# Kernel tuning notes

Measured on AMD Instinct MI355X. Metric: run time of the kernel, lower is better.

## Reference

```python
import jax, jax.numpy as jnp
import numpy as np

N, E, B, D, F_IN, E_IN, H = 8192, 32768, 256, 64, 11, 5, 128


def setup_inputs() -> dict:
    key = jax.random.key(0)
    ks = jax.random.split(key, 32)
    rn = lambda k, shape, s: jax.random.normal(k, shape, jnp.float32) * s
    inp = {
        'x': jax.random.normal(ks[0], (N, F_IN), jnp.float32),
        'edge_attr': jax.random.uniform(ks[1], (E, E_IN), jnp.float32),
        'lin0_w': rn(ks[2], (D, F_IN), 0.3), 'lin0_b': jnp.zeros((D,), jnp.float32),
        'nn1_w': rn(ks[3], (H, E_IN), 0.4), 'nn1_b': jnp.zeros((H,), jnp.float32),
        'nn2_w': rn(ks[4], (D * D, H), 0.05), 'nn2_b': jnp.zeros((D * D,), jnp.float32),
        'root_w': rn(ks[5], (D, D), 0.125), 'conv_b': jnp.zeros((D,), jnp.float32),
        'gru_w_ih': rn(ks[6], (3 * D, D), 0.125), 'gru_w_hh': rn(ks[7], (3 * D, D), 0.125),
        'gru_b_ih': jnp.zeros((3 * D,), jnp.float32), 'gru_b_hh': jnp.zeros((3 * D,), jnp.float32),
        's2s_w_ih': rn(ks[8], (4 * D, 2 * D), 0.1), 's2s_w_hh': rn(ks[9], (4 * D, D), 0.125),
        's2s_b_ih': jnp.zeros((4 * D,), jnp.float32), 's2s_b_hh': jnp.zeros((4 * D,), jnp.float32),
        'lin1_w': rn(ks[10], (D, 2 * D), 0.1), 'lin1_b': jnp.zeros((D,), jnp.float32),
        'lin2_w': rn(ks[11], (1, D), 0.125), 'lin2_b': jnp.zeros((1,), jnp.float32),
        'edge_index': jax.random.randint(ks[12], (2, E), 0, N),
        'batch': jnp.sort(jax.random.randint(ks[13], (N,), 0, B)),
    }
    return inp


def _forward(x, edge_attr, lin0_w, lin0_b, nn1_w, nn1_b, nn2_w, nn2_b, root_w, conv_b,
             gru_w_ih, gru_w_hh, gru_b_ih, gru_b_hh, s2s_w_ih, s2s_w_hh, s2s_b_ih, s2s_b_hh,
             lin1_w, lin1_b, lin2_w, lin2_b, edge_index, batch):
    src, dst = edge_index[0], edge_index[1]
    # edge-conditioned weights: MLP(edge_attr) -> [E, D, D]; edge_attr is fixed,
    # so compute once (identical math to calling conv.nn each iteration)
    W_e = (jax.nn.relu(edge_attr @ nn1_w.T + nn1_b) @ nn2_w.T + nn2_b).reshape(E, D, D)
    deg = jax.ops.segment_sum(jnp.ones((E,), jnp.float32), dst, num_segments=N)
    inv_deg = jnp.where(deg > 0, 1.0 / jnp.maximum(deg, 1.0), 0.0)[:, None]  # [N,1]

    out = jax.nn.relu(x @ lin0_w.T + lin0_b)  # [N, D]
    h = out
    for _ in range(3):
        # NNConv: gather src features, per-edge matmul, scatter-mean to dst, + root + bias
        msg = jnp.einsum('ed,edf->ef', out[src], W_e)  # [E, D]
        agg = jax.ops.segment_sum(msg, dst, num_segments=N) * inv_deg
        m = jax.nn.relu(agg + out @ root_w.T + conv_b)
        # single-step GRU (torch GRU equations)
        gx = m @ gru_w_ih.T + gru_b_ih
        gh = h @ gru_w_hh.T + gru_b_hh
        xr, xz, xn = jnp.split(gx, 3, axis=-1)
        hr, hz, hn = jnp.split(gh, 3, axis=-1)
        r = jax.nn.sigmoid(xr + hr)
        z = jax.nn.sigmoid(xz + hz)
        n = jnp.tanh(xn + r * hn)
        h = (1.0 - z) * n + z * h
        out = h

    # Set2Set pooling, 3 processing steps
    qh = jnp.zeros((B, D), jnp.float32)
    qc = jnp.zeros((B, D), jnp.float32)
    q_star = jnp.zeros((B, 2 * D), jnp.float32)
    for _ in range(3):
        gates = q_star @ s2s_w_ih.T + s2s_b_ih + qh @ s2s_w_hh.T + s2s_b_hh
        gi, gf, gg, go = jnp.split(gates, 4, axis=-1)
        qc = jax.nn.sigmoid(gf) * qc + jax.nn.sigmoid(gi) * jnp.tanh(gg)
        qh = jax.nn.sigmoid(go) * jnp.tanh(qc)
        q = qh  # [B, D]
        e = jnp.sum(out * q[batch], axis=-1)  # [N]
        emax = jax.ops.segment_max(e, batch, num_segments=B)
        emax = jnp.where(jnp.isfinite(emax), emax, 0.0)
        a = jnp.exp(e - emax[batch])
        a_sum = jax.ops.segment_sum(a, batch, num_segments=B)
        a = a / jnp.maximum(a_sum, 1e-12)[batch]
        r_vec = jax.ops.segment_sum(a[:, None] * out, batch, num_segments=B)  # [B, D]
        q_star = jnp.concatenate([q, r_vec], axis=-1)

    y = jax.nn.relu(q_star @ lin1_w.T + lin1_b) @ lin2_w.T + lin2_b
    return y.reshape(-1)  # [B]


def reference(x, edge_attr, lin0_w, lin0_b, nn1_w, nn1_b, nn2_w, nn2_b, root_w, conv_b,
              gru_w_ih, gru_w_hh, gru_b_ih, gru_b_hh, s2s_w_ih, s2s_w_hh, s2s_b_ih, s2s_b_hh,
              lin1_w, lin1_b, lin2_w, lin2_b, edge_index, batch):
    return _forward(x, edge_attr, lin0_w, lin0_b, nn1_w, nn1_b, nn2_w, nn2_b, root_w, conv_b,
                    gru_w_ih, gru_w_hh, gru_b_ih, gru_b_hh, s2s_w_ih, s2s_w_hh, s2s_b_ih, s2s_b_hh,
                    lin1_w, lin1_b, lin2_w, lin2_b, edge_index, batch)
```

## Files before the change

### kernel.cpp

```cpp
#include <hip/hip_runtime.h>
#include <hip/hip_bf16.h>
#include <stdint.h>

#define NN 8192
#define EE 32768
#define BB 256
#define DD 64
#define FIN 11
#define EIN 5
#define HH 128

typedef __attribute__((ext_vector_type(4))) float f32x4;
typedef __attribute__((ext_vector_type(8))) short bf16x8;

__device__ __forceinline__ float sigmoidf_(float x) { return 1.0f / (1.0f + expf(-x)); }

__device__ __forceinline__ void gload16(const void* g, void* l) {
    __builtin_amdgcn_global_load_lds(
        (const __attribute__((address_space(1))) unsigned int*)g,
        (__attribute__((address_space(3))) unsigned int*)l, 16, 0, 0);
}

__global__ __launch_bounds__(256) void k_cast(const float* __restrict__ src,
                                              __hip_bfloat16* __restrict__ dst) {
    int i = (blockIdx.x * 256 + threadIdx.x) * 4;
    float4 v = *(const float4*)(src + i);
    ushort4 o;
    __hip_bfloat16 b0 = __float2bfloat16(v.x); o.x = *(ushort*)&b0;
    __hip_bfloat16 b1 = __float2bfloat16(v.y); o.y = *(ushort*)&b1;
    __hip_bfloat16 b2 = __float2bfloat16(v.z); o.z = *(ushort*)&b2;
    __hip_bfloat16 b3 = __float2bfloat16(v.w); o.w = *(ushort*)&b3;
    *(ushort4*)((ushort*)dst + i) = o;
}

__global__ __launch_bounds__(256) void k_prep(const float* __restrict__ root_w,
                                              const float* __restrict__ whh,
                                              const float* __restrict__ bhh,
                                              const float* __restrict__ nn2b,
                                              float* __restrict__ Bcat,
                                              float* __restrict__ bcat) {
    int i = blockIdx.x * 256 + threadIdx.x;
    int r = i >> 6, c = i & 63;
    float v;
    if (r < 64) v = root_w[i];
    else if (r < 256) v = whh[(size_t)(r - 64) * 64 + c];
    else v = nn2b[c * 64 + (r - 256)];
    Bcat[i] = v;
    if (c == 0) bcat[r] = (r >= 64 && r < 256) ? bhh[r - 64] : 0.0f;
}

__global__ __launch_bounds__(256) void k_tw(const float* __restrict__ wih,
                                            const float* __restrict__ whh,
                                            float* __restrict__ wihT,
                                            float* __restrict__ whhT) {
    int i = blockIdx.x * 256 + threadIdx.x;
    if (i < 256 * 128) {
        int j = i >> 7, k = i & 127;
        wihT[k * 256 + j] = wih[i];
    } else {
        int i2 = i - 256 * 128;
        if (i2 < 256 * 64) {
            int j = i2 >> 6, k = i2 & 63;
            whhT[k * 256 + j] = whh[i2];
        }
    }
}

__global__ __launch_bounds__(256) void k_lin0(const float* __restrict__ x,
                                              const float* __restrict__ w,
                                              const float* __restrict__ b,
                                              float* __restrict__ out) {
    int idx = blockIdx.x * 256 + threadIdx.x;
    int n = idx >> 6, d = idx & 63;
    float a = b[d];
#pragma unroll
    for (int k = 0; k < FIN; k++) a += x[n * FIN + k] * w[d * FIN + k];
    out[idx] = fmaxf(a, 0.0f);
}

__global__ __launch_bounds__(256) void k_h1(const float* __restrict__ ea,
                                            const float* __restrict__ w,
                                            const float* __restrict__ b,
                                            __hip_bfloat16* __restrict__ h1) {
    int idx = blockIdx.x * 256 + threadIdx.x;
    int e = idx >> 7, k = idx & 127;
    float a = b[k];
#pragma unroll
    for (int j = 0; j < EIN; j++) a += ea[e * EIN + j] * w[k * EIN + j];
    h1[idx] = __float2bfloat16(fmaxf(a, 0.0f));
}

__global__ __launch_bounds__(256) void k_counts(const int* __restrict__ ei,
                                                const int* __restrict__ batch,
                                                int* __restrict__ deg,
                                                int* __restrict__ cnt) {
    int i = blockIdx.x * 256 + threadIdx.x;
    if (i < EE) atomicAdd(&deg[ei[EE + i]], 1);
    if (i < NN) atomicAdd(&cnt[batch[i]], 1);
}
__global__ __launch_bounds__(256) void k_inv(const int* __restrict__ deg, float* __restrict__ invd) {
    int n = blockIdx.x * 256 + threadIdx.x;
    if (n < NN) { int d = deg[n]; invd[n] = d > 0 ? 1.0f / (float)d : 0.0f; }
}
__global__ __launch_bounds__(256) void k_scan(const int* __restrict__ cnt, int* __restrict__ offs) {
    __shared__ int s[256];
    int t = threadIdx.x;
    s[t] = cnt[t];
    __syncthreads();
    for (int off = 1; off < 256; off <<= 1) {
        int v = (t >= off) ? s[t - off] : 0;
        __syncthreads();
        s[t] += v;
        __syncthreads();
    }
    offs[t + 1] = s[t];
    if (t == 0) offs[0] = 0;
}

__global__ __launch_bounds__(256) void k_wemsg(const __hip_bfloat16* __restrict__ h1,
                                               const __hip_bfloat16* __restrict__ nn2bf,
                                               const float* __restrict__ outN,
                                               const float* __restrict__ rgh,
                                               const int* __restrict__ ei,
                                               const float* __restrict__ invd,
                                               float* __restrict__ agg) {
    __shared__ ushort sB[2][64 * 128];
    __shared__ float soT[64 * 64];
    __shared__ float snbT[64 * 64];
    __shared__ int sDst[64];
    __shared__ float sIv[64];

    const int t = threadIdx.x;
    const int w = t >> 6, l = t & 63;
    const int q = l >> 4, l15 = l & 15;
    const int e0 = blockIdx.x * 64;

    {
        int r = t >> 2, seg = t & 3;
        int s_ = ei[e0 + r];
        const float* orow = outN + (size_t)s_ * 64 + seg * 16;
        const float* nrow = rgh + (size_t)s_ * 320 + 256 + seg * 16;
#pragma unroll
        for (int i = 0; i < 4; i++) {
            float4 v = *(const float4*)(orow + i * 4);
            float4 nb = *(const float4*)(nrow + i * 4);
            int c0 = seg * 16 + i * 4;
            soT[(c0 + 0) * 64 + r] = v.x;
            soT[(c0 + 1) * 64 + r] = v.y;
            soT[(c0 + 2) * 64 + r] = v.z;
            soT[(c0 + 3) * 64 + r] = v.w;
            snbT[(c0 + 0) * 64 + r] = nb.x;
            snbT[(c0 + 1) * 64 + r] = nb.y;
            snbT[(c0 + 2) * 64 + r] = nb.z;
            snbT[(c0 + 3) * 64 + r] = nb.w;
        }
        if (seg == 0) {
            int d_ = ei[EE + e0 + r];
            sDst[r] = d_;
            sIv[r] = invd[d_];
        }
    }
    bf16x8 af[4][4];
#pragma unroll
    for (int mi = 0; mi < 4; mi++)
#pragma unroll
        for (int kk = 0; kk < 4; kk++)
            af[mi][kk] = *(const bf16x8*)(h1 + (size_t)(e0 + mi * 16 + l15) * 128 + (kk * 4 + q) * 8);

#pragma unroll
    for (int i = 0; i < 4; i++) {
        int u = i * 256 + t;
        int r = u >> 4, c = u & 15, cs = c ^ (r & 7);
        gload16(nn2bf + ((size_t)r * 128 + cs * 8), &sB[0][(i * 256 + w * 64) * 8]);
    }
    __syncthreads();

    float msg[4][4];
#pragma unroll
    for (int mi = 0; mi < 4; mi++)
#pragma unroll
        for (int j = 0; j < 4; j++) msg[mi][j] = 0.0f;

    for (int d = 0; d < 64; ++d) {
        const int cur = d & 1;
        if (d < 63) {
#pragma unroll
            for (int i = 0; i < 4; i++) {
                int u = i * 256 + t;
                int r = u >> 4, c = u & 15, cs = c ^ (r & 7);
                gload16(nn2bf + ((size_t)((d + 1) * 64 + r) * 128 + cs * 8),
                        &sB[cur ^ 1][(i * 256 + w * 64) * 8]);
            }
        }
        const ushort* sbc = &sB[cur][0];
        f32x4 acc[4];
#pragma unroll
        for (int mi = 0; mi < 4; mi++) acc[mi] = (f32x4)0.0f;
        const int rb = w * 16 + l15;
#pragma unroll
        for (int kk = 0; kk < 4; kk++) {
            bf16x8 bfr = *(const bf16x8*)&sbc[(rb * 16 + ((kk * 4 + q) ^ (rb & 7))) * 8];
#pragma unroll
            for (int mi = 0; mi < 4; mi++)
                acc[mi] = __builtin_amdgcn_mfma_f32_16x16x32_bf16(af[mi][kk], bfr, acc[mi], 0, 0, 0);
        }
#pragma unroll
        for (int mi = 0; mi < 4; mi++) {
            f32x4 sov = *(const f32x4*)&soT[d * 64 + mi * 16 + q * 4];
#pragma unroll
            for (int j = 0; j < 4; j++) msg[mi][j] += acc[mi][j] * sov[j];
        }
        __syncthreads();
    }

#pragma unroll
    for (int mi = 0; mi < 4; mi++) {
        f32x4 nb = *(const f32x4*)&snbT[(w * 16 + l15) * 64 + mi * 16 + q * 4];
#pragma unroll
        for (int j = 0; j < 4; j++) {
            int er = mi * 16 + q * 4 + j;
            atomicAdd(&agg[(size_t)sDst[er] * 64 + w * 16 + l15], (msg[mi][j] + nb[j]) * sIv[er]);
        }
    }
}

__global__ __launch_bounds__(256) void k_rgh(const float* __restrict__ A,
                                             const float* __restrict__ Bm,
                                             const float* __restrict__ bias,
                                             float* __restrict__ C,
                                             float* __restrict__ aggz) {
    const int tid = threadIdx.x;
    const int bx = blockIdx.x, by = blockIdx.y;
    {
        int bid = by * 5 + bx;
        if (bid < 512) {
            float4 z; z.x = z.y = z.z = z.w = 0.0f;
            *(float4*)(aggz + (size_t)bid * 1024 + tid * 4) = z;
        }
    }
    __shared__ float sA[64 * 68];
    __shared__ float sB[64 * 68];
    const float* Ab = A + (size_t)by * 64 * 64;
    const float* Bb = Bm + (size_t)bx * 64 * 64;
    for (int fi = tid; fi < 64 * 16; fi += 256) {
        int r = fi >> 4, c = (fi & 15) * 4;
        *(float4*)&sA[r * 68 + c] = *(const float4*)(Ab + (size_t)r * 64 + c);
        *(float4*)&sB[r * 68 + c] = *(const float4*)(Bb + (size_t)r * 64 + c);
    }
    __syncthreads();
    const int tx = tid & 15, ty = tid >> 4;
    float acc[4][4];
#pragma unroll
    for (int i = 0; i < 4; i++)
#pragma unroll
        for (int j = 0; j < 4; j++) acc[i][j] = 0.0f;
    for (int k = 0; k < 64; k += 4) {
        float4 av[4], bv[4];
#pragma unroll
        for (int i = 0; i < 4; i++) av[i] = *(const float4*)&sA[(ty + 16 * i) * 68 + k];
#pragma unroll
        for (int j = 0; j < 4; j++) bv[j] = *(const float4*)&sB[(tx + 16 * j) * 68 + k];
#pragma unroll
        for (int i = 0; i < 4; i++)
#pragma unroll
            for (int j = 0; j < 4; j++) {
                acc[i][j] += av[i].x * bv[j].x;
                acc[i][j] += av[i].y * bv[j].y;
                acc[i][j] += av[i].z * bv[j].z;
                acc[i][j] += av[i].w * bv[j].w;
            }
    }
#pragma unroll
    for (int i = 0; i < 4; i++) {
        size_t row = (size_t)by * 64 + ty + 16 * i;
#pragma unroll
        for (int j = 0; j < 4; j++) {
            int col = bx * 64 + tx + 16 * j;
            C[row * 320 + col] = acc[i][j] + bias[col];
        }
    }
}

__global__ __launch_bounds__(256) void k_gxgru(const float* __restrict__ agg,
                                               const float* __restrict__ rgh,
                                               const float* __restrict__ cb,
                                               const float* __restrict__ wih,
                                               const float* __restrict__ bih,
                                               float* __restrict__ outN) {
    __shared__ float sA[64 * 68];
    __shared__ float sB[192 * 68];
    const int t = threadIdx.x;
    const int by = blockIdx.x;
    for (int fi = t; fi < 64 * 16; fi += 256) {
        int r = fi >> 4, c = (fi & 15) * 4;
        float4 av = *(const float4*)(agg + (size_t)(by * 64 + r) * 64 + c);
        float4 rv = *(const float4*)(rgh + (size_t)(by * 64 + r) * 320 + c);
        float4 cv = *(const float4*)(cb + c);
        float4 m;
        m.x = fmaxf(av.x + rv.x + cv.x, 0.0f);
        m.y = fmaxf(av.y + rv.y + cv.y, 0.0f);
        m.z = fmaxf(av.z + rv.z + cv.z, 0.0f);
        m.w = fmaxf(av.w + rv.w + cv.w, 0.0f);
        *(float4*)&sA[r * 68 + c] = m;
    }
    for (int fi = t; fi < 192 * 16; fi += 256) {
        int r = fi >> 4, c = (fi & 15) * 4;
        *(float4*)&sB[r * 68 + c] = *(const float4*)(wih + (size_t)r * 64 + c);
    }
    __syncthreads();
    const int tx = t & 15, ty = t >> 4;
    float acc[3][4][4];
#pragma unroll
    for (int cx = 0; cx < 3; cx++)
#pragma unroll
        for (int i = 0; i < 4; i++)
#pragma unroll
            for (int j = 0; j < 4; j++) acc[cx][i][j] = 0.0f;
    for (int k = 0; k < 64; k += 4) {
        float4 av[4];
#pragma unroll
        for (int i = 0; i < 4; i++) av[i] = *(const float4*)&sA[(ty + 16 * i) * 68 + k];
#pragma unroll
        for (int cx = 0; cx < 3; cx++) {
            float4 bv[4];
#pragma unroll
            for (int j = 0; j < 4; j++) bv[j] = *(const float4*)&sB[(cx * 64 + tx + 16 * j) * 68 + k];
#pragma unroll
            for (int i = 0; i < 4; i++)
#pragma unroll
                for (int j = 0; j < 4; j++) {
                    acc[cx][i][j] += av[i].x * bv[j].x;
                    acc[cx][i][j] += av[i].y * bv[j].y;
                    acc[cx][i][j] += av[i].z * bv[j].z;
                    acc[cx][i][j] += av[i].w * bv[j].w;
                }
        }
    }
#pragma unroll
    for (int i = 0; i < 4; i++) {
        int n = by * 64 + ty + 16 * i;
        const float* ghr = rgh + (size_t)n * 320 + 64;
#pragma unroll
        for (int j = 0; j < 4; j++) {
            int d = tx + 16 * j;
            float r = sigmoidf_(acc[0][i][j] + bih[d] + ghr[d]);
            float z = sigmoidf_(acc[1][i][j] + bih[64 + d] + ghr[64 + d]);
            float nn_ = tanhf(acc[2][i][j] + bih[128 + d] + r * ghr[128 + d]);
            float hp = outN[(size_t)n * 64 + d];
            outN[(size_t)n * 64 + d] = (1.0f - z) * nn_ + z * hp;
        }
    }
}

__global__ __launch_bounds__(256) void k_s2sall(const float* __restrict__ outN,
                                                const int* __restrict__ offs,
                                                const float* __restrict__ wihT,
                                                const float* __restrict__ whhT,
                                                const float* __restrict__ bih,
                                                const float* __restrict__ bhh,
                                                const float* __restrict__ lin1_w,
                                                const float* __restrict__ lin1_b,
                                                const float* __restrict__ lin2_w,
                                                const float* __restrict__ lin2_b,
                                                float* __restrict__ earr,
                                                float* __restrict__ y) {
    const int b = blockIdx.x, t = threadIdx.x;
    const int w = t >> 6, l = t & 63;
    __shared__ float qs[128], qhL[64], qcL[64], gates[256];
    __shared__ float red[8];
    __shared__ float rpart[4][64];
    __shared__ float hbuf[64];
    const int s0 = offs[b], s1 = offs[b + 1];
    if (t < 128) qs[t] = 0.0f;
    if (t < 64) { qhL[t] = 0.0f; qcL[t] = 0.0f; }
    __syncthreads();

    for (int st = 0; st < 3; st++) {
        float g = bih[t] + bhh[t];
        for (int k = 0; k < 128; k++) g += qs[k] * wihT[k * 256 + t];
        for (int k = 0; k < 64; k++) g += qhL[k] * whhT[k * 256 + t];
        gates[t] = g;
        __syncthreads();
        if (t < 64) {
            float gi = gates[t], gf = gates[64 + t], gg = gates[128 + t], go = gates[192 + t];
            float c = sigmoidf_(gf) * qcL[t] + sigmoidf_(gi) * tanhf(gg);
            qcL[t] = c;
            qhL[t] = sigmoidf_(go) * tanhf(c);
        }
        __syncthreads();
        float mx = -INFINITY;
        for (int i = s0 + w; i < s1; i += 4) {
            float p = outN[(size_t)i * 64 + l] * qhL[l];
#pragma unroll
            for (int o = 32; o > 0; o >>= 1) p += __shfl_xor(p, o, 64);
            if (l == 0) earr[i] = p;
            mx = fmaxf(mx, p);
        }
        if (l == 0) red[w] = mx;
        __syncthreads();
        mx = fmaxf(fmaxf(red[0], red[1]), fmaxf(red[2], red[3]));
        if (!isfinite(mx)) mx = 0.0f;
        float sm = 0.0f, racc = 0.0f;
        for (int i = s0 + w; i < s1; i += 4) {
            float a = expf(earr[i] - mx);
            sm += a;
            racc += a * outN[(size_t)i * 64 + l];
        }
        rpart[w][l] = racc;
        if (l == 0) red[4 + w] = sm;
        __syncthreads();
        float smT = fmaxf(red[4] + red[5] + red[6] + red[7], 1e-12f);
        if (t < 64) {
            float r = (rpart[0][t] + rpart[1][t] + rpart[2][t] + rpart[3][t]) / smT;
            qs[t] = qhL[t];
            qs[64 + t] = r;
        }
        __syncthreads();
    }
    if (t < 64) {
        float h = lin1_b[t];
        for (int k = 0; k < 128; k++) h += qs[k] * lin1_w[t * 128 + k];
        hbuf[t] = fmaxf(h, 0.0f) * lin2_w[t];
    }
    __syncthreads();
    if (w == 0) {
        float p = hbuf[l];
#pragma unroll
        for (int o = 32; o > 0; o >>= 1) p += __shfl_xor(p, o, 64);
        if (l == 0) y[b] = p + lin2_b[0];
    }
}

extern "C" void kernel_launch(void* const* d_in, const int* in_sizes, int n_in,
                              void* d_out, int out_size, void* d_ws, size_t ws_size,
                              hipStream_t stream) {
    const float* x = (const float*)d_in[0];
    const float* edge_attr = (const float*)d_in[1];
    const float* lin0_w = (const float*)d_in[2];
    const float* lin0_b = (const float*)d_in[3];
    const float* nn1_w = (const float*)d_in[4];
    const float* nn1_b = (const float*)d_in[5];
    const float* nn2_w = (const float*)d_in[6];
    const float* nn2_b = (const float*)d_in[7];
    const float* root_w = (const float*)d_in[8];
    const float* conv_b = (const float*)d_in[9];
    const float* gru_w_ih = (const float*)d_in[10];
    const float* gru_w_hh = (const float*)d_in[11];
    const float* gru_b_ih = (const float*)d_in[12];
    const float* gru_b_hh = (const float*)d_in[13];
    const float* s2s_w_ih = (const float*)d_in[14];
    const float* s2s_w_hh = (const float*)d_in[15];
    const float* s2s_b_ih = (const float*)d_in[16];
    const float* s2s_b_hh = (const float*)d_in[17];
    const float* lin1_w = (const float*)d_in[18];
    const float* lin1_b = (const float*)d_in[19];
    const float* lin2_w = (const float*)d_in[20];
    const float* lin2_b = (const float*)d_in[21];
    const int* ei = (const int*)d_in[22];
    const int* batch = (const int*)d_in[23];
    float* outp = (float*)d_out;

    char* w = (char*)d_ws;
    auto carve = [&](size_t bytes) { char* p = w; w += (bytes + 255) & ~(size_t)255; return p; };
    __hip_bfloat16* nn2bf = (__hip_bfloat16*)carve((size_t)4096 * 128 * 2);
    float* outN = (float*)carve((size_t)NN * 64 * 4);
    __hip_bfloat16* h1 = (__hip_bfloat16*)carve((size_t)EE * 128 * 2);
    int* deg = (int*)carve(NN * 4);
    float* invd = (float*)carve(NN * 4);
    float* agg = (float*)carve((size_t)NN * 64 * 4);
    float* rgh = (float*)carve((size_t)NN * 320 * 4);
    float* Bcat = (float*)carve((size_t)320 * 64 * 4);
    float* bcat = (float*)carve(320 * 4);
    float* wihT = (float*)carve((size_t)128 * 256 * 4);
    float* whhT = (float*)carve((size_t)64 * 256 * 4);
    float* earr = (float*)carve(NN * 4);
    int* cnt = (int*)carve(256 * 4);
    int* offs = (int*)carve(257 * 4);

    hipMemsetAsync(deg, 0, NN * 4, stream);
    hipMemsetAsync(cnt, 0, 256 * 4, stream);

    k_cast<<<512, 256, 0, stream>>>(nn2_w, nn2bf);
    k_prep<<<80, 256, 0, stream>>>(root_w, gru_w_hh, gru_b_hh, nn2_b, Bcat, bcat);
    k_tw<<<192, 256, 0, stream>>>(s2s_w_ih, s2s_w_hh, wihT, whhT);
    k_lin0<<<NN * 64 / 256, 256, 0, stream>>>(x, lin0_w, lin0_b, outN);
    k_h1<<<EE * 128 / 256, 256, 0, stream>>>(edge_attr, nn1_w, nn1_b, h1);
    k_counts<<<EE / 256, 256, 0, stream>>>(ei, batch, deg, cnt);
    k_inv<<<NN / 256, 256, 0, stream>>>(deg, invd);
    k_scan<<<1, 256, 0, stream>>>(cnt, offs);

    for (int it = 0; it < 3; it++) {
        k_rgh<<<dim3(5, NN / 64), 256, 0, stream>>>(outN, Bcat, bcat, rgh, agg);
        k_wemsg<<<EE / 64, 256, 0, stream>>>(h1, nn2bf, outN, rgh, ei, invd, agg);
        k_gxgru<<<NN / 64, 256, 0, stream>>>(agg, rgh, conv_b, gru_w_ih, gru_b_ih, outN);
    }

    k_s2sall<<<BB, 256, 0, stream>>>(outN, offs, wihT, whhT, s2s_b_ih, s2s_b_hh,
                                     lin1_w, lin1_b, lin2_w, lin2_b, earr, outp);
}
```

Measured before the change: 347.8 us.

## Load edge-MLP weight fragments directly from global memory, dropping LDS staging

In the per-edge message kernel, the nn2 weight tiles are now read straight from global memory into registers instead of being staged through a double-buffered LDS array with async global-to-LDS loads. This removes the per-iteration barrier and the LDS traffic, and the loop is unrolled by four so independent loads can overlap with MFMA work. In exchange, every block re-reads the 1 MB weight matrix through the cache with no LDS reuse, and load latency is exposed unless the unrolling hides it.

```diff
diff --git a/kernel.cpp b/kernel.cpp
--- a/kernel.cpp
+++ b/kernel.cpp
@@ -14,12 +14,6 @@
 typedef __attribute__((ext_vector_type(8))) short bf16x8;
 
 __device__ __forceinline__ float sigmoidf_(float x) { return 1.0f / (1.0f + expf(-x)); }
-
-__device__ __forceinline__ void gload16(const void* g, void* l) {
-    __builtin_amdgcn_global_load_lds(
-        (const __attribute__((address_space(1))) unsigned int*)g,
-        (__attribute__((address_space(3))) unsigned int*)l, 16, 0, 0);
-}
 
 __global__ __launch_bounds__(256) void k_cast(const float* __restrict__ src,
                                               __hip_bfloat16* __restrict__ dst) {
@@ -124,7 +118,6 @@
                                                const int* __restrict__ ei,
                                                const float* __restrict__ invd,
                                                float* __restrict__ agg) {
-    __shared__ ushort sB[2][64 * 128];
     __shared__ float soT[64 * 64];
     __shared__ float snbT[64 * 64];
     __shared__ int sDst[64];
@@ -166,13 +159,6 @@
 #pragma unroll
         for (int kk = 0; kk < 4; kk++)
             af[mi][kk] = *(const bf16x8*)(h1 + (size_t)(e0 + mi * 16 + l15) * 128 + (kk * 4 + q) * 8);
-
-#pragma unroll
-    for (int i = 0; i < 4; i++) {
-        int u = i * 256 + t;
-        int r = u >> 4, c = u & 15, cs = c ^ (r & 7);
-        gload16(nn2bf + ((size_t)r * 128 + cs * 8), &sB[0][(i * 256 + w * 64) * 8]);
-    }
     __syncthreads();
 
     float msg[4][4];
@@ -181,36 +167,28 @@
 #pragma unroll
         for (int j = 0; j < 4; j++) msg[mi][j] = 0.0f;
 
+    const __hip_bfloat16* bp = nn2bf + (size_t)(w * 16 + l15) * 128 + q * 8;
+
+#pragma unroll 4
     for (int d = 0; d < 64; ++d) {
-        const int cur = d & 1;
-        if (d < 63) {
-#pragma unroll
-            for (int i = 0; i < 4; i++) {
-                int u = i * 256 + t;
-                int r = u >> 4, c = u & 15, cs = c ^ (r & 7);
-                gload16(nn2bf + ((size_t)((d + 1) * 64 + r) * 128 + cs * 8),
-                        &sB[cur ^ 1][(i * 256 + w * 64) * 8]);
-            }
-        }
-        const ushort* sbc = &sB[cur][0];
+        bf16x8 bfr[4];
+#pragma unroll
+        for (int kk = 0; kk < 4; kk++)
+            bfr[kk] = *(const bf16x8*)(bp + (size_t)d * 8192 + kk * 32);
         f32x4 acc[4];
 #pragma unroll
         for (int mi = 0; mi < 4; mi++) acc[mi] = (f32x4)0.0f;
-        const int rb = w * 16 + l15;
-#pragma unroll
-        for (int kk = 0; kk < 4; kk++) {
-            bf16x8 bfr = *(const bf16x8*)&sbc[(rb * 16 + ((kk * 4 + q) ^ (rb & 7))) * 8];
+#pragma unroll
+        for (int kk = 0; kk < 4; kk++)
 #pragma unroll
             for (int mi = 0; mi < 4; mi++)
-                acc[mi] = __builtin_amdgcn_mfma_f32_16x16x32_bf16(af[mi][kk], bfr, acc[mi], 0, 0, 0);
-        }
+                acc[mi] = __builtin_amdgcn_mfma_f32_16x16x32_bf16(af[mi][kk], bfr[kk], acc[mi], 0, 0, 0);
 #pragma unroll
         for (int mi = 0; mi < 4; mi++) {
             f32x4 sov = *(const f32x4*)&soT[d * 64 + mi * 16 + q * 4];
 #pragma unroll
             for (int j = 0; j < 4; j++) msg[mi][j] += acc[mi][j] * sov[j];
         }
-        __syncthreads();
     }
 
 #pragma unroll
```

New measurement: 380.5 us. +9.4%, slower.
